# Kernel optimization log

Measured on AMD Instinct MI355X. Metric: run time of the kernel, lower is better.

The kernel has to match this reference:

```python
import jax, jax.numpy as jnp
import numpy as np

IN_F = 128
OUT_F = 128
GROUPS = 8
NUM_F = 8
B = 16
NP_ = 4096


def setup_inputs() -> dict:
    key = jax.random.key(0)
    ks = jax.random.split(key, 6)
    x = jax.random.normal(ks[0], (B, NP_, IN_F), dtype=jnp.float32)
    grid = jnp.arange(NUM_F, dtype=jnp.float32) + 1.0                      # [num_f]
    base_weight = jax.random.normal(ks[1], (OUT_F, IN_F), dtype=jnp.float32) * 0.05
    scale_sp = jnp.ones((OUT_F,), dtype=jnp.float32)
    coef = jax.random.uniform(ks[2], (GROUPS, 1, NUM_F), dtype=jnp.float32)
    conv_w = jax.random.normal(ks[3], (NUM_F, OUT_F, IN_F), dtype=jnp.float32) * 0.05  # grouped 1x1 conv
    conv_b = jax.random.normal(ks[4], (NUM_F, OUT_F), dtype=jnp.float32) * 0.05
    return {"x": x, "grid": grid, "base_weight": base_weight,
            "scale_sp": scale_sp, "coef": coef, "conv_w": conv_w, "conv_b": conv_b}


def reference(x, grid, base_weight, scale_sp, coef, conv_w, conv_b):
    Bd, Nd, D = x.shape
    num_f = grid.shape[0]
    groups = coef.shape[0]
    gsz = D // groups
    xf = x.reshape(Bd * Nd, D)                                  # [batch, in]
    # base path: SiLU then linear (no bias)
    base = jax.nn.silu(xf) @ base_weight.T                       # [batch, out]
    # spline path: sin(grid * x), broadcast coef per (group, f)
    s = jnp.sin(grid[None, :, None] * xf[:, None, :])            # [batch, num_f, in]
    cm = coef[:, 0, :].T                                         # [num_f, groups]
    s = s.reshape(-1, num_f, groups, gsz) * cm[None, :, :, None]
    s = s.reshape(-1, num_f, D)                                  # [batch, num_f, in]
    # grouped 1x1 conv == per-f GEMM
    spline = jnp.einsum('bfi,foi->bfo', s, conv_w) + conv_b[None]
    spline = spline.sum(axis=1) * scale_sp                       # [batch, out]
    out = (base + spline).reshape(Bd, Nd, -1)
    return out
```

## Files before the change

### kernel.cpp

```cpp
#include <hip/hip_runtime.h>
#include <hip/hip_bf16.h>
#include <stdint.h>

#define IN_F   128
#define OUT_F  128
#define NUM_F  8
#define NROWS  (16*4096)

typedef __bf16  bf16x8  __attribute__((ext_vector_type(8)));
typedef float   f32x16  __attribute__((ext_vector_type(16)));

#define WP_CHUNKS (9*8*4*64)

__device__ __bf16 g_Wp[WP_CHUNKS * 8];
__device__ float  g_bias[OUT_F];

__global__ __launch_bounds__(256) void skan_prep(
    const float* __restrict__ base_w,
    const float* __restrict__ scale,
    const float* __restrict__ coef,
    const float* __restrict__ conv_w,
    const float* __restrict__ conv_b)
{
    int gid = blockIdx.x * 256 + threadIdx.x;
    int l  = gid & 63;
    int t  = (gid >> 6) & 3;
    int s  = (gid >> 8) & 7;
    int fb = gid >> 11;
    int n  = t * 32 + (l & 31);
    int k0 = s * 16 + (l >> 5) * 8;
    __bf16* dst = g_Wp + (size_t)gid * 8;
    if (fb == 0) {
        #pragma unroll
        for (int j = 0; j < 8; ++j)
            dst[j] = (__bf16)base_w[n * IN_F + k0 + j];
    } else {
        int f = fb - 1;
        float sc = scale[n];
        #pragma unroll
        for (int j = 0; j < 8; ++j) {
            int k = k0 + j;
            float v = conv_w[((size_t)f * OUT_F + n) * IN_F + k]
                      * coef[(k >> 4) * NUM_F + f] * sc;
            dst[j] = (__bf16)v;
        }
    }
    if (gid < OUT_F) {
        float b = 0.f;
        #pragma unroll
        for (int f = 0; f < NUM_F; ++f) b += conv_b[f * OUT_F + gid];
        g_bias[gid] = b * scale[gid];
    }
}

__device__ __forceinline__ void gld_lds16(const void* g, void* l) {
    __builtin_amdgcn_global_load_lds(
        (const __attribute__((address_space(1))) uint32_t*)g,
        (__attribute__((address_space(3))) uint32_t*)l, 16, 0, 0);
}

__global__ __launch_bounds__(256, 2) void skan_main(
    const float* __restrict__ x,
    float* __restrict__ out)
{
    __shared__ uint4 smem4[2048];
    char* smem = (char*)smem4;

    const int tid = threadIdx.x;
    const int w   = tid >> 6;
    const int l   = tid & 63;
    const int hl  = l & 31;
    const int h   = l >> 5;
    const int m0  = blockIdx.x * 128 + w * 32;
    const int m   = m0 + hl;

    const float4* x4 = (const float4*)x + (size_t)m * (IN_F / 4) + 2 * h;
    float xe[64];
    #pragma unroll
    for (int s = 0; s < 8; ++s) {
        float4 a = x4[4 * s];
        float4 b = x4[4 * s + 1];
        xe[8*s+0] = a.x; xe[8*s+1] = a.y; xe[8*s+2] = a.z; xe[8*s+3] = a.w;
        xe[8*s+4] = b.x; xe[8*s+5] = b.y; xe[8*s+6] = b.z; xe[8*s+7] = b.w;
    }

    f32x16 acc[4];
    #pragma unroll
    for (int t = 0; t < 4; ++t)
        #pragma unroll
        for (int r = 0; r < 16; ++r) acc[t][r] = 0.f;

    const bf16x8* bp = (const bf16x8*)smem;
    const char* wpb  = (const char*)g_Wp;

    for (int fb = 0; fb < 9; ++fb) {
        __syncthreads();
        {
            const char* src = wpb + (size_t)fb * 32768;
            #pragma unroll
            for (int r = 0; r < 8; ++r) {
                int off = (r * 4 + w) * 1024;
                gld_lds16(src + off + l * 16, smem + off);
            }
        }
        bf16x8 af[8];
        if (fb == 0) {
            #pragma unroll
            for (int s = 0; s < 8; ++s)
                #pragma unroll
                for (int j = 0; j < 8; ++j) {
                    float v = xe[8*s+j];
                    float sv = v * __builtin_amdgcn_rcpf(1.0f + __expf(-v));
                    af[s][j] = (__bf16)sv;
                }
        } else {
            float cf = (float)fb * 0.15915494309189535f;
            #pragma unroll
            for (int s = 0; s < 8; ++s)
                #pragma unroll
                for (int j = 0; j < 8; ++j) {
                    float a = __builtin_amdgcn_fractf(cf * xe[8*s+j]);
                    af[s][j] = (__bf16)__builtin_amdgcn_sinf(a);
                }
        }
        __syncthreads();
        #pragma unroll
        for (int s = 0; s < 8; ++s) {
            #pragma unroll
            for (int t = 0; t < 4; ++t) {
                bf16x8 b = bp[(s * 4 + t) * 64 + l];
                acc[t] = __builtin_amdgcn_mfma_f32_32x32x16_bf16(af[s], b, acc[t], 0, 0, 0);
            }
        }
    }

    #pragma unroll
    for (int t = 0; t < 4; ++t) {
        float bv = g_bias[t * 32 + hl];
        #pragma unroll
        for (int r = 0; r < 16; ++r) {
            int row = (r & 3) + 8 * (r >> 2) + 4 * h;
            out[(size_t)(m0 + row) * OUT_F + t * 32 + hl] = acc[t][r] + bv;
        }
    }
}

extern "C" void kernel_launch(void* const* d_in, const int* in_sizes, int n_in,
                              void* d_out, int out_size, void* d_ws, size_t ws_size,
                              hipStream_t stream) {
    const float* x      = (const float*)d_in[0];
    const float* base_w = (const float*)d_in[2];
    const float* scale  = (const float*)d_in[3];
    const float* coef   = (const float*)d_in[4];
    const float* conv_w = (const float*)d_in[5];
    const float* conv_b = (const float*)d_in[6];
    float* out = (float*)d_out;
    (void)d_ws; (void)ws_size;

    skan_prep<<<WP_CHUNKS / 256, 256, 0, stream>>>(base_w, scale, coef, conv_w, conv_b);
    skan_main<<<NROWS / 128, 256, 0, stream>>>(x, out);
}
```

Measured before the change: 113.7 us.

## Double-buffer weight tiles in LDS with async prefetch and manual waitcnt

Doubles the LDS weight buffer to 64KB so the next feature block's weights are prefetched via global_load_lds while the current block runs MFMAs. The two full __syncthreads per block become manual vmcnt waits plus raw barriers. The activations (SiLU or sin) are now computed per k-slice, interleaved with the MFMAs, instead of being materialised up front. The larger LDS footprint may reduce occupancy below two blocks per CU, and the vmcnt counts depend on how the compiler orders its loads.

```diff
diff --git a/kernel.cpp b/kernel.cpp
--- a/kernel.cpp
+++ b/kernel.cpp
@@ -12,7 +12,7 @@
 
 #define WP_CHUNKS (9*8*4*64)
 
-__device__ __bf16 g_Wp[WP_CHUNKS * 8];
+__device__ __attribute__((aligned(256))) __bf16 g_Wp[WP_CHUNKS * 8];
 __device__ float  g_bias[OUT_F];
 
 __global__ __launch_bounds__(256) void skan_prep(
@@ -63,7 +63,7 @@
     const float* __restrict__ x,
     float* __restrict__ out)
 {
-    __shared__ uint4 smem4[2048];
+    __shared__ uint4 smem4[4096];
     char* smem = (char*)smem4;
 
     const int tid = threadIdx.x;
@@ -73,6 +73,20 @@
     const int h   = l >> 5;
     const int m0  = blockIdx.x * 128 + w * 32;
     const int m   = m0 + hl;
+
+    const char* wpb = (const char*)g_Wp;
+
+    #pragma unroll
+    for (int r = 0; r < 8; ++r) {
+        int off = (r * 4 + w) * 1024;
+        gld_lds16(wpb + off + l * 16, smem + off);
+    }
+    #pragma unroll
+    for (int r = 0; r < 8; ++r) {
+        int off = (r * 4 + w) * 1024;
+        gld_lds16(wpb + 32768 + off + l * 16, smem + 32768 + off);
+    }
+    asm volatile("" ::: "memory");
 
     const float4* x4 = (const float4*)x + (size_t)m * (IN_F / 4) + 2 * h;
     float xe[64];
@@ -90,46 +104,66 @@
         #pragma unroll
         for (int r = 0; r < 16; ++r) acc[t][r] = 0.f;
 
-    const bf16x8* bp = (const bf16x8*)smem;
-    const char* wpb  = (const char*)g_Wp;
+    asm volatile("s_waitcnt vmcnt(24)" ::: "memory");
+    __builtin_amdgcn_s_barrier();
+    asm volatile("" ::: "memory");
+    {
+        const bf16x8* bp = (const bf16x8*)smem;
+        #pragma unroll
+        for (int s = 0; s < 8; ++s) {
+            bf16x8 af;
+            #pragma unroll
+            for (int j = 0; j < 8; ++j) {
+                float v = xe[8*s+j];
+                float sv = v * __builtin_amdgcn_rcpf(1.0f + __expf(-v));
+                af[j] = (__bf16)sv;
+            }
+            #pragma unroll
+            for (int t = 0; t < 4; ++t) {
+                bf16x8 b = bp[(s * 4 + t) * 64 + l];
+                acc[t] = __builtin_amdgcn_mfma_f32_32x32x16_bf16(af, b, acc[t], 0, 0, 0);
+            }
+        }
+    }
+    asm volatile("" ::: "memory");
+    __builtin_amdgcn_s_barrier();
+    #pragma unroll
+    for (int r = 0; r < 8; ++r) {
+        int off = (r * 4 + w) * 1024;
+        gld_lds16(wpb + 2 * 32768 + off + l * 16, smem + off);
+    }
 
-    for (int fb = 0; fb < 9; ++fb) {
-        __syncthreads();
-        {
-            const char* src = wpb + (size_t)fb * 32768;
+    for (int fb = 1; fb <= 8; ++fb) {
+        if (fb < 8) asm volatile("s_waitcnt vmcnt(8)" ::: "memory");
+        else        asm volatile("s_waitcnt vmcnt(0)" ::: "memory");
+        __builtin_amdgcn_s_barrier();
+        asm volatile("" ::: "memory");
+
+        const bf16x8* bp = (const bf16x8*)(smem + (fb & 1) * 32768);
+        float cf = (float)fb * 0.15915494309189535f;
+        #pragma unroll
+        for (int s = 0; s < 8; ++s) {
+            bf16x8 af;
+            #pragma unroll
+            for (int j = 0; j < 8; ++j) {
+                float a = __builtin_amdgcn_fractf(cf * xe[8*s+j]);
+                af[j] = (__bf16)__builtin_amdgcn_sinf(a);
+            }
+            #pragma unroll
+            for (int t = 0; t < 4; ++t) {
+                bf16x8 b = bp[(s * 4 + t) * 64 + l];
+                acc[t] = __builtin_amdgcn_mfma_f32_32x32x16_bf16(af, b, acc[t], 0, 0, 0);
+            }
+        }
+
+        if (fb <= 6) {
+            asm volatile("" ::: "memory");
+            __builtin_amdgcn_s_barrier();
             #pragma unroll
             for (int r = 0; r < 8; ++r) {
                 int off = (r * 4 + w) * 1024;
-                gld_lds16(src + off + l * 16, smem + off);
-            }
-        }
-        bf16x8 af[8];
-        if (fb == 0) {
-            #pragma unroll
-            for (int s = 0; s < 8; ++s)
-                #pragma unroll
-                for (int j = 0; j < 8; ++j) {
-                    float v = xe[8*s+j];
-                    float sv = v * __builtin_amdgcn_rcpf(1.0f + __expf(-v));
-                    af[s][j] = (__bf16)sv;
-                }
-        } else {
-            float cf = (float)fb * 0.15915494309189535f;
-            #pragma unroll
-            for (int s = 0; s < 8; ++s)
-                #pragma unroll
-                for (int j = 0; j < 8; ++j) {
-                    float a = __builtin_amdgcn_fractf(cf * xe[8*s+j]);
-                    af[s][j] = (__bf16)__builtin_amdgcn_sinf(a);
-                }
-        }
-        __syncthreads();
-        #pragma unroll
-        for (int s = 0; s < 8; ++s) {
-            #pragma unroll
-            for (int t = 0; t < 4; ++t) {
-                bf16x8 b = bp[(s * 4 + t) * 64 + l];
-                acc[t] = __builtin_amdgcn_mfma_f32_32x32x16_bf16(af[s], b, acc[t], 0, 0, 0);
+                gld_lds16(wpb + (size_t)(fb + 2) * 32768 + off + l * 16,
+                          smem + (fb & 1) * 32768 + off);
             }
         }
     }
```

New measurement: 113.5 us. No clear change (-0.2%).

## Reorder K-loop by input slice with double-buffered weights and Chebyshev sine recurrence

Applied to the files above, without the earlier changes.

The weight layout now groups all nine feature blocks for each 16-wide K slice, and the main loop iterates over K slices instead of feature blocks. Weight tiles are double-buffered in LDS, with manual vmcnt waits and x loads prefetched two slices ahead. sin(k·x) for k=2..8 comes from a Chebyshev recurrence seeded by one sin and one cos, instead of eight separate sin evaluations. This cuts transcendental work and overlaps loads with MFMA, but raises LDS use to 72KB per block, which may lower occupancy, and adds small numerical drift from the recurrence.

```diff
diff --git a/kernel.cpp b/kernel.cpp
--- a/kernel.cpp
+++ b/kernel.cpp
@@ -9,10 +9,12 @@
 
 typedef __bf16  bf16x8  __attribute__((ext_vector_type(8)));
 typedef float   f32x16  __attribute__((ext_vector_type(16)));
+typedef float   f32x4   __attribute__((ext_vector_type(4)));
 
-#define WP_CHUNKS (9*8*4*64)
+#define WP_CHUNKS (8*9*4*64)
+#define SBLK      36864
 
-__device__ __bf16 g_Wp[WP_CHUNKS * 8];
+__device__ __attribute__((aligned(256))) __bf16 g_Wp[WP_CHUNKS * 8];
 __device__ float  g_bias[OUT_F];
 
 __global__ __launch_bounds__(256) void skan_prep(
@@ -25,8 +27,9 @@
     int gid = blockIdx.x * 256 + threadIdx.x;
     int l  = gid & 63;
     int t  = (gid >> 6) & 3;
-    int s  = (gid >> 8) & 7;
-    int fb = gid >> 11;
+    int r  = gid >> 8;
+    int s  = r / 9;
+    int fb = r % 9;
     int n  = t * 32 + (l & 31);
     int k0 = s * 16 + (l >> 5) * 8;
     __bf16* dst = g_Wp + (size_t)gid * 8;
@@ -63,7 +66,7 @@
     const float* __restrict__ x,
     float* __restrict__ out)
 {
-    __shared__ uint4 smem4[2048];
+    __shared__ uint4 smem4[4608];
     char* smem = (char*)smem4;
 
     const int tid = threadIdx.x;
@@ -74,15 +77,17 @@
     const int m0  = blockIdx.x * 128 + w * 32;
     const int m   = m0 + hl;
 
-    const float4* x4 = (const float4*)x + (size_t)m * (IN_F / 4) + 2 * h;
-    float xe[64];
+    const char* wpb = (const char*)g_Wp;
+
     #pragma unroll
-    for (int s = 0; s < 8; ++s) {
-        float4 a = x4[4 * s];
-        float4 b = x4[4 * s + 1];
-        xe[8*s+0] = a.x; xe[8*s+1] = a.y; xe[8*s+2] = a.z; xe[8*s+3] = a.w;
-        xe[8*s+4] = b.x; xe[8*s+5] = b.y; xe[8*s+6] = b.z; xe[8*s+7] = b.w;
-    }
+    for (int r = 0; r < 9; ++r)
+        gld_lds16(wpb + (r * 256 + tid) * 16, smem + (r * 256 + tid) * 16);
+    asm volatile("" ::: "memory");
+
+    const f32x4* x4 = (const f32x4*)x + (size_t)m * (IN_F / 4) + 2 * h;
+    f32x4 xa[8], xb[8];
+    xa[0] = x4[0]; xb[0] = x4[1];
+    xa[1] = x4[4]; xb[1] = x4[5];
 
     f32x16 acc[4];
     #pragma unroll
@@ -90,48 +95,51 @@
         #pragma unroll
         for (int r = 0; r < 16; ++r) acc[t][r] = 0.f;
 
-    const bf16x8* bp = (const bf16x8*)smem;
-    const char* wpb  = (const char*)g_Wp;
+    #pragma unroll
+    for (int s = 0; s < 8; ++s) {
+        if (s < 7) asm volatile("s_waitcnt vmcnt(2)" ::: "memory");
+        else       asm volatile("s_waitcnt vmcnt(0)" ::: "memory");
+        __builtin_amdgcn_s_barrier();
 
-    for (int fb = 0; fb < 9; ++fb) {
-        __syncthreads();
-        {
-            const char* src = wpb + (size_t)fb * 32768;
+        if (s < 7) {
+            const char* src = wpb + (size_t)(s + 1) * SBLK;
+            char*       dst = smem + ((s + 1) & 1) * SBLK;
             #pragma unroll
-            for (int r = 0; r < 8; ++r) {
-                int off = (r * 4 + w) * 1024;
-                gld_lds16(src + off + l * 16, smem + off);
+            for (int r = 0; r < 9; ++r)
+                gld_lds16(src + (r * 256 + tid) * 16, dst + (r * 256 + tid) * 16);
+        }
+        asm volatile("" ::: "memory");
+        if (s < 6) { xa[s + 2] = x4[4 * (s + 2)]; xb[s + 2] = x4[4 * (s + 2) + 1]; }
+
+        bf16x8 af[9];
+        #pragma unroll
+        for (int j = 0; j < 8; ++j) {
+            float v = (j < 4) ? xa[s][j] : xb[s][j - 4];
+            float sv = v * __builtin_amdgcn_rcpf(1.0f + __expf(-v));
+            af[0][j] = (__bf16)sv;
+            float u  = __builtin_amdgcn_fractf(v * 0.15915494309189535f);
+            float s1 = __builtin_amdgcn_sinf(u);
+            float c2 = 2.0f * __builtin_amdgcn_cosf(u);
+            af[1][j] = (__bf16)s1;
+            float sp = s1;
+            float sc = c2 * s1;
+            af[2][j] = (__bf16)sc;
+            #pragma unroll
+            for (int f = 3; f <= 8; ++f) {
+                float sn = c2 * sc - sp;
+                af[f][j] = (__bf16)sn;
+                sp = sc; sc = sn;
             }
         }
-        bf16x8 af[8];
-        if (fb == 0) {
-            #pragma unroll
-            for (int s = 0; s < 8; ++s)
-                #pragma unroll
-                for (int j = 0; j < 8; ++j) {
-                    float v = xe[8*s+j];
-                    float sv = v * __builtin_amdgcn_rcpf(1.0f + __expf(-v));
-                    af[s][j] = (__bf16)sv;
-                }
-        } else {
-            float cf = (float)fb * 0.15915494309189535f;
-            #pragma unroll
-            for (int s = 0; s < 8; ++s)
-                #pragma unroll
-                for (int j = 0; j < 8; ++j) {
-                    float a = __builtin_amdgcn_fractf(cf * xe[8*s+j]);
-                    af[s][j] = (__bf16)__builtin_amdgcn_sinf(a);
-                }
-        }
-        __syncthreads();
+
+        const bf16x8* bp = (const bf16x8*)(smem + (s & 1) * SBLK);
         #pragma unroll
-        for (int s = 0; s < 8; ++s) {
+        for (int fb = 0; fb < 9; ++fb)
             #pragma unroll
             for (int t = 0; t < 4; ++t) {
-                bf16x8 b = bp[(s * 4 + t) * 64 + l];
-                acc[t] = __builtin_amdgcn_mfma_f32_32x32x16_bf16(af[s], b, acc[t], 0, 0, 0);
+                bf16x8 b = bp[(fb * 4 + t) * 64 + l];
+                acc[t] = __builtin_amdgcn_mfma_f32_32x32x16_bf16(af[fb], b, acc[t], 0, 0, 0);
             }
-        }
     }
 
     #pragma unroll
```

After: 109.0 us, median of 2. -4.2%, faster.
